# Kernel optimization log

Hardware: AMD Instinct MI355X
Metric: run time of the kernel (lower is better)

Reference implementation:

```python
import jax, jax.numpy as jnp
import numpy as np

TOP_K = 8  # num_experts_per_tok


def setup_inputs() -> dict:
    key = jax.random.key(0)
    k1, k2, k3 = jax.random.split(key, 3)
    B, S, H, E = 4, 4096, 2048, 64
    hidden_states = jax.random.normal(k1, (B, S, H), dtype=jnp.float32)
    router_weight = jax.random.normal(k2, (E, H), dtype=jnp.float32)
    router_bias = jnp.zeros((E,), dtype=jnp.float32)
    expert_bias = jax.random.normal(k3, (E, H), dtype=jnp.float32) * 0.1
    return {
        "hidden_states": hidden_states,
        "router_weight": router_weight,
        "router_bias": router_bias,
        "expert_bias": expert_bias,
    }


def reference(hidden_states, router_weight, router_bias, expert_bias):
    B, S, H = hidden_states.shape
    flat = hidden_states.reshape(B * S, H)  # [T, H]
    # Router: linear -> softmax -> top-k
    logits = jnp.einsum("th,eh->te", flat, router_weight) + router_bias
    scores = jax.nn.softmax(logits, axis=-1)
    topk_w, topk_idx = jax.lax.top_k(scores, TOP_K)  # [T, K]
    # Dispatch/combine collapses to: combined[t,k] = x[t] + expert_bias[idx[t,k]]
    # output[t] = sum_k w[t,k] * combined[t,k]
    #          = x[t] * sum_k w[t,k] + sum_k w[t,k] * expert_bias[idx[t,k]]
    gathered_bias = expert_bias[topk_idx]  # [T, K, H]
    out = flat * jnp.sum(topk_w, axis=-1, keepdims=True) + jnp.einsum(
        "tk,tkh->th", topk_w, gathered_bias
    )
    return out.reshape(B, S, H)
```

## Files before the change

kernel.cpp:

```cpp
#include <hip/hip_runtime.h>
#include <hip/hip_bf16.h>
#include <float.h>

#define H 2048
#define E 64
#define TOPK 8
#define TT 8
#define NT 512

typedef __attribute__((ext_vector_type(8))) short bf16x8;
typedef __attribute__((ext_vector_type(4))) float f32x4;
typedef __attribute__((ext_vector_type(4))) unsigned short us4;

__device__ __forceinline__ unsigned short f2bf(float f) {
  unsigned u = __float_as_uint(f);
  u += 0x7fffu + ((u >> 16) & 1u);
  return (unsigned short)(u >> 16);
}
__device__ __forceinline__ float bf2f(unsigned short s) {
  return __uint_as_float(((unsigned)s) << 16);
}
__device__ __forceinline__ float wred_max(float v) {
#pragma unroll
  for (int o = 32; o > 0; o >>= 1) v = fmaxf(v, __shfl_xor(v, o));
  return v;
}
__device__ __forceinline__ float wred_sum(float v) {
#pragma unroll
  for (int o = 32; o > 0; o >>= 1) v += __shfl_xor(v, o);
  return v;
}

__global__ __launch_bounds__(256) void cvt_kernel(const float* __restrict__ W,
                                                  const float* __restrict__ eb,
                                                  unsigned short* __restrict__ Wb,
                                                  unsigned short* __restrict__ Bb) {
  int i = (blockIdx.x * 256 + threadIdx.x) * 4;
  const float* src;
  unsigned short* dst;
  int off;
  if (i < E * H) { src = W; dst = Wb; off = i; }
  else           { src = eb; dst = Bb; off = i - E * H; }
  float4 v = *(const float4*)(src + off);
  us4 r;
  r[0] = f2bf(v.x); r[1] = f2bf(v.y); r[2] = f2bf(v.z); r[3] = f2bf(v.w);
  *(us4*)(dst + off) = r;
}

template <bool USE_WS>
__global__ __launch_bounds__(NT, 8) void moe_kernel(
    const float* __restrict__ x, const float* __restrict__ W,
    const float* __restrict__ rb, const float* __restrict__ eb,
    const unsigned short* __restrict__ Wb, const unsigned short* __restrict__ Bb,
    float* __restrict__ out) {
  __shared__ unsigned short xl[TT][H + 8];
  __shared__ float lgp[2][TT][E + 1];
  __shared__ float msw[TT];
  __shared__ float mw[TT][TOPK];
  __shared__ int   mi[TT][TOPK];

  const int tid = threadIdx.x;
  const int t0  = blockIdx.x * TT;
  const int wv = tid >> 6, lane = tid & 63, quad = lane >> 4, m = lane & 15;

  {
    const float* row = x + (size_t)(t0 + wv) * H;
#pragma unroll
    for (int i = 0; i < 8; ++i) {
      const int c = (i * 64 + lane) * 4;
      float4 a = *(const float4*)(row + c);
      us4 ra;
      ra[0] = f2bf(a.x); ra[1] = f2bf(a.y); ra[2] = f2bf(a.z); ra[3] = f2bf(a.w);
      *(us4*)&xl[wv][c] = ra;
    }
  }
  __syncthreads();

  {
    const int eg = wv & 3, kh = wv >> 2;
    const int e = eg * 16 + m;
    const int k0 = kh * (H / 2);
    f32x4 acc = {0.f, 0.f, 0.f, 0.f};
    const unsigned short* xp = &xl[m & 7][k0 + quad * 8];
    if (USE_WS) {
      const unsigned short* wp = Wb + (size_t)e * H + k0 + quad * 8;
#pragma unroll 8
      for (int it = 0; it < H / 64; ++it) {
        bf16x8 av = *(const bf16x8*)(xp + it * 32);
        bf16x8 bv = *(const bf16x8*)(wp + it * 32);
        acc = __builtin_amdgcn_mfma_f32_16x16x32_bf16(av, bv, acc, 0, 0, 0);
      }
    } else {
      const float* wp = W + (size_t)e * H + k0 + quad * 8;
#pragma unroll 4
      for (int it = 0; it < H / 64; ++it) {
        bf16x8 av = *(const bf16x8*)(xp + it * 32);
        float4 p = *(const float4*)(wp + it * 32);
        float4 q = *(const float4*)(wp + it * 32 + 4);
        bf16x8 bv;
        bv[0] = (short)f2bf(p.x); bv[1] = (short)f2bf(p.y);
        bv[2] = (short)f2bf(p.z); bv[3] = (short)f2bf(p.w);
        bv[4] = (short)f2bf(q.x); bv[5] = (short)f2bf(q.y);
        bv[6] = (short)f2bf(q.z); bv[7] = (short)f2bf(q.w);
        acc = __builtin_amdgcn_mfma_f32_16x16x32_bf16(av, bv, acc, 0, 0, 0);
      }
    }
#pragma unroll
    for (int r = 0; r < 4; ++r) {
      const int row = quad * 4 + r;
      if (row < TT) lgp[kh][row][eg * 16 + m] = acc[r];
    }
  }
  __syncthreads();

  {
    const int t = wv;
    float l = lgp[0][t][lane] + lgp[1][t][lane] + rb[lane];
    const float mx = wred_max(l);
    const float p = expf(l - mx);
    const float inv = 1.f / wred_sum(p);
    float sumw = 0.f;
    float lsel = l;
#pragma unroll
    for (int k = 0; k < TOPK; ++k) {
      const float mk = wred_max(lsel);
      const unsigned long long b = __ballot(lsel == mk);
      const int idx = __ffsll(b) - 1;
      const float wk = expf(mk - mx) * inv;
      sumw += wk;
      if (lane == 0) { mw[t][k] = wk; mi[t][k] = idx * H; }
      if (lane == idx) lsel = -FLT_MAX;
    }
    if (lane == 0) msw[t] = sumw;
  }
  __syncthreads();

  {
    const int tg = tid >> 8;
    const int c8 = (tid & 255) * 8;
    const unsigned short* bbase = Bb + c8;
    const float* ebase = eb + c8;
#pragma unroll 1
    for (int tt = 0; tt < TT / 2; ++tt) {
      const int t = tg * (TT / 2) + tt;
      const float sw = msw[t];
      const float4 w0 = *(const float4*)&mw[t][0];
      const float4 w1 = *(const float4*)&mw[t][4];
      const int4  e0 = *(const int4*)&mi[t][0];
      const int4  e1 = *(const int4*)&mi[t][4];
      const float wks[8] = {w0.x, w0.y, w0.z, w0.w, w1.x, w1.y, w1.z, w1.w};
      const int   ofs[8] = {e0.x, e0.y, e0.z, e0.w, e1.x, e1.y, e1.z, e1.w};
      bf16x8 xv = *(const bf16x8*)&xl[t][c8];
      float o[8];
#pragma unroll
      for (int i = 0; i < 8; ++i) o[i] = bf2f((unsigned short)xv[i]) * sw;
#pragma unroll
      for (int k = 0; k < TOPK; ++k) {
        const float wk = wks[k];
        if (USE_WS) {
          bf16x8 bv = *(const bf16x8*)(bbase + ofs[k]);
#pragma unroll
          for (int i = 0; i < 8; ++i) o[i] += wk * bf2f((unsigned short)bv[i]);
        } else {
          const float* p = ebase + ofs[k];
          float4 p0 = *(const float4*)p;
          float4 p1 = *(const float4*)(p + 4);
          o[0] += wk * p0.x; o[1] += wk * p0.y; o[2] += wk * p0.z; o[3] += wk * p0.w;
          o[4] += wk * p1.x; o[5] += wk * p1.y; o[6] += wk * p1.z; o[7] += wk * p1.w;
        }
      }
      float* op = out + (size_t)(t0 + t) * H + c8;
      *(float4*)op       = make_float4(o[0], o[1], o[2], o[3]);
      *(float4*)(op + 4) = make_float4(o[4], o[5], o[6], o[7]);
    }
  }
}

extern "C" void kernel_launch(void* const* d_in, const int* in_sizes, int n_in,
                              void* d_out, int out_size, void* d_ws, size_t ws_size,
                              hipStream_t stream) {
  const float* x  = (const float*)d_in[0];
  const float* W  = (const float*)d_in[1];
  const float* rb = (const float*)d_in[2];
  const float* eb = (const float*)d_in[3];
  float* out = (float*)d_out;

  const int T = in_sizes[0] / H;
  const int grid = T / TT;

  const size_t need = (size_t)2 * E * H * sizeof(unsigned short);
  if (ws_size >= need) {
    unsigned short* Wb = (unsigned short*)d_ws;
    unsigned short* Bb = Wb + E * H;
    cvt_kernel<<<(2 * E * H) / (256 * 4), 256, 0, stream>>>(W, eb, Wb, Bb);
    moe_kernel<true><<<grid, NT, 0, stream>>>(x, W, rb, eb, Wb, Bb, out);
  } else {
    moe_kernel<false><<<grid, NT, 0, stream>>>(x, W, rb, eb, nullptr, nullptr, out);
  }
}
```

Measured before the change: 289.3 us.

## Split fused MoE kernel into separate router and combine kernels

Replaces the single fused kernel with a router kernel that computes logits via MFMA over 16-token tiles per wave and writes top-k weights/indices to workspace, followed by a combine kernel that re-reads x and gathers bf16 expert biases. This removes LDS staging and block-wide syncs and raises occupancy, at the cost of reading x from global memory twice and an extra launch plus metadata round-trip. The output now uses full fp32 x rather than the bf16-rounded copy. Falls back to the old fused kernel if workspace is too small.

```diff
diff --git a/kernel.cpp b/kernel.cpp
--- a/kernel.cpp
+++ b/kernel.cpp
@@ -5,6 +5,7 @@
 #define H 2048
 #define E 64
 #define TOPK 8
+#define RT 16
 #define TT 8
 #define NT 512
 
@@ -45,6 +46,108 @@
   us4 r;
   r[0] = f2bf(v.x); r[1] = f2bf(v.y); r[2] = f2bf(v.z); r[3] = f2bf(v.w);
   *(us4*)(dst + off) = r;
+}
+
+__global__ __launch_bounds__(256, 4) void router_kernel(
+    const float* __restrict__ x, const unsigned short* __restrict__ Wb,
+    const float* __restrict__ rb, float* __restrict__ msw_g,
+    float* __restrict__ mw_g, int* __restrict__ mi_g) {
+  __shared__ float lgs[4][RT][E + 1];
+  const int tid = threadIdx.x;
+  const int wv = tid >> 6, lane = tid & 63, quad = lane >> 4, m = lane & 15;
+  const int t0 = (blockIdx.x * 4 + wv) * RT;
+
+  f32x4 acc0 = {0.f,0.f,0.f,0.f}, acc1 = {0.f,0.f,0.f,0.f};
+  f32x4 acc2 = {0.f,0.f,0.f,0.f}, acc3 = {0.f,0.f,0.f,0.f};
+  const float* xp = x + (size_t)(t0 + m) * H + quad * 8;
+  const unsigned short* wp = Wb + (size_t)m * H + quad * 8;
+#pragma unroll 4
+  for (int it = 0; it < H / 32; ++it) {
+    float4 p = *(const float4*)(xp + it * 32);
+    float4 q = *(const float4*)(xp + it * 32 + 4);
+    bf16x8 av;
+    av[0] = (short)f2bf(p.x); av[1] = (short)f2bf(p.y);
+    av[2] = (short)f2bf(p.z); av[3] = (short)f2bf(p.w);
+    av[4] = (short)f2bf(q.x); av[5] = (short)f2bf(q.y);
+    av[6] = (short)f2bf(q.z); av[7] = (short)f2bf(q.w);
+    bf16x8 b0 = *(const bf16x8*)(wp + (size_t)0 * 16 * H + it * 32);
+    bf16x8 b1 = *(const bf16x8*)(wp + (size_t)1 * 16 * H + it * 32);
+    bf16x8 b2 = *(const bf16x8*)(wp + (size_t)2 * 16 * H + it * 32);
+    bf16x8 b3 = *(const bf16x8*)(wp + (size_t)3 * 16 * H + it * 32);
+    acc0 = __builtin_amdgcn_mfma_f32_16x16x32_bf16(av, b0, acc0, 0, 0, 0);
+    acc1 = __builtin_amdgcn_mfma_f32_16x16x32_bf16(av, b1, acc1, 0, 0, 0);
+    acc2 = __builtin_amdgcn_mfma_f32_16x16x32_bf16(av, b2, acc2, 0, 0, 0);
+    acc3 = __builtin_amdgcn_mfma_f32_16x16x32_bf16(av, b3, acc3, 0, 0, 0);
+  }
+#pragma unroll
+  for (int r = 0; r < 4; ++r) {
+    const int row = quad * 4 + r;
+    lgs[wv][row][ 0 + m] = acc0[r];
+    lgs[wv][row][16 + m] = acc1[r];
+    lgs[wv][row][32 + m] = acc2[r];
+    lgs[wv][row][48 + m] = acc3[r];
+  }
+  const float rbl = rb[lane];
+  for (int t = 0; t < RT; ++t) {
+    float l = lgs[wv][t][lane] + rbl;
+    const float mx = wred_max(l);
+    const float p = expf(l - mx);
+    const float inv = 1.f / wred_sum(p);
+    float sumw = 0.f, lsel = l;
+    float mywk = 0.f;
+    int myoff = 0;
+#pragma unroll
+    for (int k = 0; k < TOPK; ++k) {
+      const float mk = wred_max(lsel);
+      const unsigned long long b = __ballot(lsel == mk);
+      const int idx = __ffsll(b) - 1;
+      const float wk = expf(mk - mx) * inv;
+      sumw += wk;
+      if (lane == k) { mywk = wk; myoff = idx * H; }
+      if (lane == idx) lsel = -FLT_MAX;
+    }
+    const int tt = t0 + t;
+    if (lane == 0) msw_g[tt] = sumw;
+    if (lane < TOPK) {
+      mw_g[(size_t)tt * TOPK + lane] = mywk;
+      mi_g[(size_t)tt * TOPK + lane] = myoff;
+    }
+  }
+}
+
+__global__ __launch_bounds__(256, 4) void combine_kernel(
+    const float* __restrict__ x, const unsigned short* __restrict__ Bb,
+    const float* __restrict__ msw_g, const float* __restrict__ mw_g,
+    const int* __restrict__ mi_g, float* __restrict__ out) {
+  const int tid = threadIdx.x;
+  const int wv = tid >> 6, lane = tid & 63;
+  const int t = blockIdx.x * 4 + wv;
+  const float sw = msw_g[t];
+  const float4 w0 = *(const float4*)(mw_g + (size_t)t * TOPK);
+  const float4 w1 = *(const float4*)(mw_g + (size_t)t * TOPK + 4);
+  const int4  e0 = *(const int4*)(mi_g + (size_t)t * TOPK);
+  const int4  e1 = *(const int4*)(mi_g + (size_t)t * TOPK + 4);
+  const float wks[8] = {w0.x, w0.y, w0.z, w0.w, w1.x, w1.y, w1.z, w1.w};
+  const int   ofs[8] = {e0.x, e0.y, e0.z, e0.w, e1.x, e1.y, e1.z, e1.w};
+  const float* xr = x + (size_t)t * H;
+  float* orow = out + (size_t)t * H;
+#pragma unroll
+  for (int ch = 0; ch < 4; ++ch) {
+    const int c8 = ch * 512 + lane * 8;
+    const float4 xa = *(const float4*)(xr + c8);
+    const float4 xb = *(const float4*)(xr + c8 + 4);
+    float o[8] = {xa.x * sw, xa.y * sw, xa.z * sw, xa.w * sw,
+                  xb.x * sw, xb.y * sw, xb.z * sw, xb.w * sw};
+#pragma unroll
+    for (int k = 0; k < TOPK; ++k) {
+      const bf16x8 bv = *(const bf16x8*)(Bb + ofs[k] + c8);
+      const float wk = wks[k];
+#pragma unroll
+      for (int i = 0; i < 8; ++i) o[i] += wk * bf2f((unsigned short)bv[i]);
+    }
+    *(float4*)(orow + c8)     = make_float4(o[0], o[1], o[2], o[3]);
+    *(float4*)(orow + c8 + 4) = make_float4(o[4], o[5], o[6], o[7]);
+  }
 }
 
 template <bool USE_WS>
@@ -186,15 +289,26 @@
   float* out = (float*)d_out;
 
   const int T = in_sizes[0] / H;
-  const int grid = T / TT;
-
-  const size_t need = (size_t)2 * E * H * sizeof(unsigned short);
-  if (ws_size >= need) {
+  const size_t szW = (size_t)E * H * sizeof(unsigned short);
+  const size_t need_old = 2 * szW;
+  const size_t meta_sz = (size_t)T * 4 + (size_t)T * TOPK * 4 * 2;
+  const size_t need_new = 2 * szW + meta_sz;
+
+  if (ws_size >= need_new) {
     unsigned short* Wb = (unsigned short*)d_ws;
-    unsigned short* Bb = Wb + E * H;
+    unsigned short* Bb = Wb + (size_t)E * H;
+    float* msw_g = (float*)(Bb + (size_t)E * H);
+    float* mw_g  = msw_g + T;
+    int*   mi_g  = (int*)(mw_g + (size_t)T * TOPK);
     cvt_kernel<<<(2 * E * H) / (256 * 4), 256, 0, stream>>>(W, eb, Wb, Bb);
-    moe_kernel<true><<<grid, NT, 0, stream>>>(x, W, rb, eb, Wb, Bb, out);
+    router_kernel<<<T / (4 * RT), 256, 0, stream>>>(x, Wb, rb, msw_g, mw_g, mi_g);
+    combine_kernel<<<T / 4, 256, 0, stream>>>(x, Bb, msw_g, mw_g, mi_g, out);
+  } else if (ws_size >= need_old) {
+    unsigned short* Wb = (unsigned short*)d_ws;
+    unsigned short* Bb = Wb + (size_t)E * H;
+    cvt_kernel<<<(2 * E * H) / (256 * 4), 256, 0, stream>>>(W, eb, Wb, Bb);
+    moe_kernel<true><<<T / TT, NT, 0, stream>>>(x, W, rb, eb, Wb, Bb, out);
   } else {
-    moe_kernel<false><<<grid, NT, 0, stream>>>(x, W, rb, eb, nullptr, nullptr, out);
-  }
-}
+    moe_kernel<false><<<T / TT, NT, 0, stream>>>(x, W, rb, eb, nullptr, nullptr, out);
+  }
+}
```

After: 330.7 us. +14.3%, slower.
